# Performance work log

Hardware: AMD Instinct MI355X
Metric: run time of the kernel (lower is better)

The kernel has to match this reference:

```python
import jax, jax.numpy as jnp
import numpy as np

N_NODES = 50000
N_EDGES = 800000   # avg degree ~16
IN_CH = 128
HID = 64


def setup_inputs() -> dict:
    key = jax.random.key(0)
    k0, k1, k2, k3 = jax.random.split(key, 4)
    x = jax.random.normal(k0, (N_NODES, IN_CH), dtype=jnp.float32)
    edge_index = jax.random.randint(k1, (2, N_EDGES), 0, N_NODES, dtype=jnp.int32)
    # Glorot-ish init like torch GCNConv
    W1 = jax.random.normal(k2, (IN_CH, HID), dtype=jnp.float32) / np.sqrt(IN_CH).astype(np.float32)
    b1 = jnp.zeros((HID,), dtype=jnp.float32)
    W2 = jax.random.normal(k3, (HID, HID), dtype=jnp.float32) / np.sqrt(HID).astype(np.float32)
    b2 = jnpp = jnp.zeros((HID,), dtype=jnp.float32)
    return {"x": x, "edge_index": edge_index, "W1": W1, "b1": b1, "W2": W2, "b2": b2}


def gcn_conv(x, src, dst, W, b, n):
    """GCNConv with self-loops already appended to (src, dst).
    out = D^{-1/2} (A + I) D^{-1/2} (x @ W) + b, symmetric normalization."""
    h = x @ W                                        # [N, out]
    deg = jax.ops.segment_sum(jnp.ones(src.shape, jnp.float32), dst, num_segments=n)
    dinv = jax.lax.rsqrt(jnp.maximum(deg, 1.0))      # deg >= 1 due to self-loops
    norm = dinv[src] * dinv[dst]                     # [E+N]
    msg = h[src] * norm[:, None]                     # gather + scale
    return jax.ops.segment_sum(msg, dst, num_segments=n) + b


def reference(x, edge_index, W1, b1, W2, b2):
    n = x.shape[0]
    loop = jnp.arange(n, dtype=edge_index.dtype)
    src = jnp.concatenate([edge_index[0], loop])     # add self-loops
    dst = jnp.concatenate([edge_index[1], loop])
    # encode: GCNConv -> ReLU -> GCNConv
    z = jax.nn.relu(gcn_conv(x, src, dst, W1, b1, n))
    z = gcn_conv(z, src, dst, W2, b2, n)
    # decode: gather endpoint embeddings, elementwise product, reduce over hidden
    return (z[edge_index[0]] * z[edge_index[1]]).sum(axis=1)   # [E]
```

## Files before the change

kernel.cpp:

```cpp
#include <hip/hip_runtime.h>
#include <hip/hip_fp16.h>

#define INCH 128
#define HIDC 64
#define CAP  64

typedef int            v4i __attribute__((ext_vector_type(4)));
typedef float          v4f __attribute__((ext_vector_type(4)));
typedef unsigned int   v4u __attribute__((ext_vector_type(4)));

__device__ inline float2 u2f(unsigned int u) {
    return __half22float2(__builtin_bit_cast(__half2, u));
}
__device__ inline unsigned int f2u(float a, float b) {
    __half2 h = __float22half2_rn(make_float2(a, b));
    return __builtin_bit_cast(unsigned int, h);
}

__global__ __launch_bounds__(128, 2) void build_gemm1_kernel(const int* __restrict__ src,
                                                             const int* __restrict__ dst,
                                                             int* __restrict__ count,
                                                             unsigned short* __restrict__ col,
                                                             const float* __restrict__ x,
                                                             const float* __restrict__ W,
                                                             __half* __restrict__ hs,
                                                             int E, int N, int GB) {
    int b = (int)blockIdx.x;
    if (b >= GB) {
        int eb = b - GB;
        int g = eb & 7;
        int chunkBase = (eb >> 3) * 2048;
        int t = (int)threadIdx.x;
        if (chunkBase + 2048 <= E) {
            v4i s4[4], d4[4];
            #pragma unroll
            for (int i = 0; i < 4; ++i) {
                int e0 = chunkBase + (i * 128 + t) * 4;
                d4[i] = *(const v4i*)(dst + e0);
                s4[i] = *(const v4i*)(src + e0);
            }
            #pragma unroll
            for (int i = 0; i < 4; ++i) {
                #pragma unroll
                for (int k = 0; k < 4; ++k) {
                    int d = d4[i][k];
                    if (((d >> 4) & 7) == g) {
                        int r = atomicAdd(&count[d], 1);
                        if (r < CAP) col[(size_t)d * CAP + r] = (unsigned short)s4[i][k];
                    }
                }
            }
        } else {
            #pragma unroll
            for (int i = 0; i < 4; ++i) {
                int e0 = chunkBase + (i * 128 + t) * 4;
                for (int e = e0; e < e0 + 4 && e < E; ++e) {
                    int d = dst[e];
                    if (((d >> 4) & 7) == g) {
                        int r = atomicAdd(&count[d], 1);
                        if (r < CAP) col[(size_t)d * CAP + r] = (unsigned short)src[e];
                    }
                }
            }
        }
    } else {
        int node = (b >> 1) * 128 + (int)threadIdx.x;
        int ch0 = (b & 1) * 32;
        if (node >= N) return;
        const float4* xr = (const float4*)(x + (size_t)node * INCH);
        float acc[32];
        #pragma unroll
        for (int c = 0; c < 32; ++c) acc[c] = 0.f;
        for (int kc = 0; kc < INCH / 4; ++kc) {
            float4 xk = xr[kc];
            const float* wr = W + (kc * 4) * HIDC + ch0;
            #pragma unroll
            for (int ch = 0; ch < 32; ++ch) acc[ch] = fmaf(xk.x, wr[ch], acc[ch]);
            #pragma unroll
            for (int ch = 0; ch < 32; ++ch) acc[ch] = fmaf(xk.y, wr[HIDC + ch], acc[ch]);
            #pragma unroll
            for (int ch = 0; ch < 32; ++ch) acc[ch] = fmaf(xk.z, wr[2 * HIDC + ch], acc[ch]);
            #pragma unroll
            for (int ch = 0; ch < 32; ++ch) acc[ch] = fmaf(xk.w, wr[3 * HIDC + ch], acc[ch]);
        }
        v4u hv[4];
        #pragma unroll
        for (int k = 0; k < 4; ++k) {
            #pragma unroll
            for (int e = 0; e < 4; ++e) {
                int c2 = k * 4 + e;
                hv[k][e] = f2u(acc[2 * c2], acc[2 * c2 + 1]);
            }
        }
        v4u* hr = (v4u*)(hs + (size_t)node * HIDC + ch0);
        #pragma unroll
        for (int k = 0; k < 4; ++k) hr[k] = hv[k];
    }
}

__global__ __launch_bounds__(256) void agg1_gemm2_kernel(const int* __restrict__ count,
                                                         const unsigned short* __restrict__ col,
                                                         const __half* __restrict__ hs,
                                                         const float* __restrict__ b1,
                                                         const float* __restrict__ W2,
                                                         __half* __restrict__ out, int N) {
    __shared__ float sW2[HIDC * HIDC];
    __shared__ float sAgg[32][68];
    int t = (int)threadIdx.x;
    {
        const float4* w4 = (const float4*)W2;
        float4* s4 = (float4*)sW2;
        #pragma unroll
        for (int i = 0; i < 4; ++i) s4[t + 256 * i] = w4[t + 256 * i];
    }
    __syncthreads();

    int g = t >> 3;
    int q = t & 7;
    int node = (int)blockIdx.x * 32 + g;
    if (node >= N) return;
    int cnt = count[node];
    int deg = cnt < CAP ? cnt : CAP;
    float dn = rsqrtf((float)cnt + 1.0f);
    const v4u* z8 = (const v4u*)hs;
    v4u sf = z8[(size_t)node * 8 + q];
    float2 acc[4];
    #pragma unroll
    for (int j = 0; j < 4; ++j) {
        float2 f = u2f(sf[j]);
        acc[j] = make_float2(f.x * dn, f.y * dn);
    }
    const unsigned short* row = col + (size_t)node * CAP;
    for (int jb = 0; jb < deg; jb += 16) {
        int s[16]; int cv[16]; v4u a[16];
        #pragma unroll
        for (int u = 0; u < 16; ++u) {
            int idx = jb + u;
            s[u] = row[idx < deg ? idx : jb];
        }
        #pragma unroll
        for (int u = 0; u < 16; ++u)
            a[u] = z8[(size_t)s[u] * 8 + q];
        #pragma unroll
        for (int u = 0; u < 16; ++u)
            cv[u] = count[s[u]];
        #pragma unroll
        for (int u = 0; u < 16; ++u) {
            if (jb + u < deg) {
                float w = rsqrtf((float)cv[u] + 1.0f);
                #pragma unroll
                for (int j = 0; j < 4; ++j) {
                    float2 f = u2f(a[u][j]);
                    acc[j].x = fmaf(f.x, w, acc[j].x);
                    acc[j].y = fmaf(f.y, w, acc[j].y);
                }
            }
        }
    }
    int ch0 = q * 8;
    v4f bA = *(const v4f*)(b1 + ch0);
    v4f bB = *(const v4f*)(b1 + ch0 + 4);
    v4f pA, pB;
    #pragma unroll
    for (int j = 0; j < 4; ++j) {
        float px = fmaxf(fmaf(acc[j].x, dn, (j < 2 ? bA[2*j]   : bB[2*j-4])),   0.f);
        float py = fmaxf(fmaf(acc[j].y, dn, (j < 2 ? bA[2*j+1] : bB[2*j-3])),  0.f);
        if (j < 2) { pA[2*j] = px; pA[2*j+1] = py; }
        else       { pB[2*j-4] = px; pB[2*j-3] = py; }
    }
    *(v4f*)(&sAgg[g][ch0])     = pA;
    *(v4f*)(&sAgg[g][ch0 + 4]) = pB;
    __asm__ volatile("s_waitcnt lgkmcnt(0)" ::: "memory");

    float o[8];
    #pragma unroll
    for (int c = 0; c < 8; ++c) o[c] = 0.f;
    const float* aRow = sAgg[g];
    #pragma unroll
    for (int kk = 0; kk < 16; ++kk) {
        v4f a4 = *(const v4f*)(aRow + kk * 4);
        #pragma unroll
        for (int kv = 0; kv < 4; ++kv) {
            float av = a4[kv];
            v4f wA = *(const v4f*)(sW2 + (kk * 4 + kv) * HIDC + ch0);
            v4f wB = *(const v4f*)(sW2 + (kk * 4 + kv) * HIDC + ch0 + 4);
            #pragma unroll
            for (int c = 0; c < 4; ++c) o[c]     = fmaf(av, wA[c], o[c]);
            #pragma unroll
            for (int c = 0; c < 4; ++c) o[c + 4] = fmaf(av, wB[c], o[c + 4]);
        }
    }
    v4u hv;
    #pragma unroll
    for (int j = 0; j < 4; ++j) hv[j] = f2u(o[2*j] * dn, o[2*j+1] * dn);
    ((v4u*)out)[(size_t)node * 8 + q] = hv;
}

__global__ __launch_bounds__(256) void aggregate_kernel(const int* __restrict__ count,
                                                        const unsigned short* __restrict__ col,
                                                        const __half* __restrict__ hs,
                                                        const float* __restrict__ bias,
                                                        __half* __restrict__ agg, int N) {
    int t = (int)threadIdx.x;
    int g = t >> 3;
    int q = t & 7;
    int node = (int)blockIdx.x * 32 + g;
    if (node >= N) return;
    int cnt = count[node];
    int deg = cnt < CAP ? cnt : CAP;
    float dn = rsqrtf((float)cnt + 1.0f);
    const v4u* z8 = (const v4u*)hs;
    v4u sf = z8[(size_t)node * 8 + q];
    float2 acc[4];
    #pragma unroll
    for (int j = 0; j < 4; ++j) acc[j] = u2f(sf[j]);
    const unsigned short* row = col + (size_t)node * CAP;
    for (int jb = 0; jb < deg; jb += 16) {
        int s[16]; v4u a[16];
        #pragma unroll
        for (int u = 0; u < 16; ++u) {
            int idx = jb + u;
            s[u] = row[idx < deg ? idx : jb];
        }
        #pragma unroll
        for (int u = 0; u < 16; ++u)
            a[u] = z8[(size_t)s[u] * 8 + q];
        #pragma unroll
        for (int u = 0; u < 16; ++u) {
            if (jb + u < deg) {
                #pragma unroll
                for (int j = 0; j < 4; ++j) {
                    float2 f = u2f(a[u][j]);
                    acc[j].x += f.x;
                    acc[j].y += f.y;
                }
            }
        }
    }
    int ch0 = q * 8;
    v4f bA = *(const v4f*)(bias + ch0);
    v4f bB = *(const v4f*)(bias + ch0 + 4);
    v4u hv;
    #pragma unroll
    for (int j = 0; j < 4; ++j) {
        float bx = (j < 2) ? bA[2*j]   : bB[2*j-4];
        float by = (j < 2) ? bA[2*j+1] : bB[2*j-3];
        hv[j] = f2u(fmaf(acc[j].x, dn, bx), fmaf(acc[j].y, dn, by));
    }
    ((v4u*)agg)[(size_t)node * 8 + q] = hv;
}

__global__ __launch_bounds__(256) void decode_kernel(const int* __restrict__ src,
                                                     const int* __restrict__ dst,
                                                     const __half* __restrict__ z,
                                                     float* __restrict__ out, int E) {
    long long tid = (long long)blockIdx.x * 256 + threadIdx.x;
    int g = (int)(tid >> 3);
    int q = threadIdx.x & 7;
    int e0 = g * 8;
    if (e0 >= E) return;
    const v4u* z8 = (const v4u*)z;
    bool full = (e0 + 7 < E);
    int s[8], d[8];
    if (full) {
        v4i sv0 = __builtin_nontemporal_load((const v4i*)(src + e0));
        v4i sv1 = __builtin_nontemporal_load((const v4i*)(src + e0 + 4));
        v4i dv0 = __builtin_nontemporal_load((const v4i*)(dst + e0));
        v4i dv1 = __builtin_nontemporal_load((const v4i*)(dst + e0 + 4));
        s[0]=sv0.x; s[1]=sv0.y; s[2]=sv0.z; s[3]=sv0.w;
        s[4]=sv1.x; s[5]=sv1.y; s[6]=sv1.z; s[7]=sv1.w;
        d[0]=dv0.x; d[1]=dv0.y; d[2]=dv0.z; d[3]=dv0.w;
        d[4]=dv1.x; d[5]=dv1.y; d[6]=dv1.z; d[7]=dv1.w;
    } else {
        #pragma unroll
        for (int k = 0; k < 8; ++k) {
            int e = e0 + k < E ? e0 + k : e0;
            s[k] = src[e]; d[k] = dst[e];
        }
    }
    v4u a[8], b[8];
    #pragma unroll
    for (int k = 0; k < 8; ++k) a[k] = z8[(size_t)s[k] * 8 + q];
    #pragma unroll
    for (int k = 0; k < 8; ++k) b[k] = z8[(size_t)d[k] * 8 + q];
    float p[8];
    #pragma unroll
    for (int k = 0; k < 8; ++k) {
        float acc = 0.f;
        #pragma unroll
        for (int j = 0; j < 4; ++j) {
            float2 fa = u2f(a[k][j]);
            float2 fb = u2f(b[k][j]);
            acc = fmaf(fa.x, fb.x, acc);
            acc = fmaf(fa.y, fb.y, acc);
        }
        p[k] = acc;
    }
    #pragma unroll
    for (int m = 4; m; m >>= 1) {
        #pragma unroll
        for (int k = 0; k < 8; ++k) p[k] += __shfl_xor(p[k], m, 64);
    }
    if (q == 0) {
        if (full) {
            v4f r0; r0.x = p[0]; r0.y = p[1]; r0.z = p[2]; r0.w = p[3];
            v4f r1; r1.x = p[4]; r1.y = p[5]; r1.z = p[6]; r1.w = p[7];
            __builtin_nontemporal_store(r0, (v4f*)(out + e0));
            __builtin_nontemporal_store(r1, (v4f*)(out + e0 + 4));
        } else {
            for (int k = 0; k < 8 && e0 + k < E; ++k) out[e0 + k] = p[k];
        }
    }
}

extern "C" void kernel_launch(void* const* d_in, const int* in_sizes, int n_in,
                              void* d_out, int out_size, void* d_ws, size_t ws_size,
                              hipStream_t stream) {
    const float* x  = (const float*)d_in[0];
    const int*   ei = (const int*)d_in[1];
    const float* W1 = (const float*)d_in[2];
    const float* b1 = (const float*)d_in[3];
    const float* W2 = (const float*)d_in[4];
    const float* b2 = (const float*)d_in[5];
    float* out = (float*)d_out;

    const int hid  = in_sizes[3];
    const int inch = in_sizes[2] / hid;
    const int N    = in_sizes[0] / inch;
    const int E    = in_sizes[1] / 2;
    const int* srcp = ei;
    const int* dstp = ei + E;

    char* p = (char*)d_ws;
    auto alloc = [&](size_t bytes) { char* r = p; p += (bytes + 255) & ~(size_t)255; return r; };
    int*            count = (int*)alloc((size_t)N * 4);
    unsigned short* col   = (unsigned short*)alloc((size_t)N * CAP * 2);
    __half*         h1s   = (__half*)alloc((size_t)N * HIDC * 2);
    __half*         h2s   = (__half*)alloc((size_t)N * HIDC * 2);
    __half*         zt    = (__half*)alloc((size_t)N * HIDC * 2);

    (void)hipMemsetAsync(count, 0, (size_t)N * 4, stream);

    int GB  = 2 * ((N + 127) / 128);
    int EBK = 8 * ((E + 2047) / 2048);
    build_gemm1_kernel<<<GB + EBK, 128, 0, stream>>>(srcp, dstp, count, col,
                                                     x, W1, h1s, E, N, GB);

    agg1_gemm2_kernel<<<(N + 31) / 32, 256, 0, stream>>>(count, col, h1s, b1, W2, h2s, N);

    aggregate_kernel<<<(N + 31) / 32, 256, 0, stream>>>(count, col, h2s, b2, zt, N);

    long long groups = ((long long)E + 7) / 8;
    long long blocksD = (groups * 8 + 255) / 256;
    decode_kernel<<<(int)blocksD, 256, 0, stream>>>(srcp, dstp, zt, out, E);
}
```

Baseline: 186.5 us.

## Split hidden features into two 32-channel halves processed by separate gather passes

The node feature tables are split into two separate 32-channel half arrays (A/B), and each gather-heavy pass (aggregations and edge decode) runs once per half. Each random gather then touches a smaller working set (1.6 MB per half), so it may fit better in L2/MALL cache. The cost is more kernel launches, gathering the column indices and degree counts twice, and a read-modify-write of the output in the second decode pass. The nontemporal loads and stores in decode are also dropped.

```diff
diff --git a/kernel.cpp b/kernel.cpp
--- a/kernel.cpp
+++ b/kernel.cpp
@@ -23,7 +23,8 @@
                                                              unsigned short* __restrict__ col,
                                                              const float* __restrict__ x,
                                                              const float* __restrict__ W,
-                                                             __half* __restrict__ hs,
+                                                             __half* __restrict__ h1A,
+                                                             __half* __restrict__ h1B,
                                                              int E, int N, int GB) {
     int b = (int)blockIdx.x;
     if (b >= GB) {
@@ -92,38 +93,28 @@
                 hv[k][e] = f2u(acc[2 * c2], acc[2 * c2 + 1]);
             }
         }
-        v4u* hr = (v4u*)(hs + (size_t)node * HIDC + ch0);
+        __half* ht = (b & 1) ? h1B : h1A;
+        v4u* hr = (v4u*)(ht + (size_t)node * 32);
         #pragma unroll
         for (int k = 0; k < 4; ++k) hr[k] = hv[k];
     }
 }
 
-__global__ __launch_bounds__(256) void agg1_gemm2_kernel(const int* __restrict__ count,
-                                                         const unsigned short* __restrict__ col,
-                                                         const __half* __restrict__ hs,
-                                                         const float* __restrict__ b1,
-                                                         const float* __restrict__ W2,
-                                                         __half* __restrict__ out, int N) {
-    __shared__ float sW2[HIDC * HIDC];
-    __shared__ float sAgg[32][68];
+__global__ __launch_bounds__(256) void agg1_half_kernel(const int* __restrict__ count,
+                                                        const unsigned short* __restrict__ col,
+                                                        const __half* __restrict__ hhalf,
+                                                        const float* __restrict__ bhalf,
+                                                        __half* __restrict__ thalf, int N) {
     int t = (int)threadIdx.x;
-    {
-        const float4* w4 = (const float4*)W2;
-        float4* s4 = (float4*)sW2;
-        #pragma unroll
-        for (int i = 0; i < 4; ++i) s4[t + 256 * i] = w4[t + 256 * i];
-    }
-    __syncthreads();
-
-    int g = t >> 3;
-    int q = t & 7;
-    int node = (int)blockIdx.x * 32 + g;
+    int g = t >> 2;
+    int q = t & 3;
+    int node = (int)blockIdx.x * 64 + g;
     if (node >= N) return;
     int cnt = count[node];
     int deg = cnt < CAP ? cnt : CAP;
     float dn = rsqrtf((float)cnt + 1.0f);
-    const v4u* z8 = (const v4u*)hs;
-    v4u sf = z8[(size_t)node * 8 + q];
+    const v4u* z4 = (const v4u*)hhalf;
+    v4u sf = z4[(size_t)node * 4 + q];
     float2 acc[4];
     #pragma unroll
     for (int j = 0; j < 4; ++j) {
@@ -140,7 +131,7 @@
         }
         #pragma unroll
         for (int u = 0; u < 16; ++u)
-            a[u] = z8[(size_t)s[u] * 8 + q];
+            a[u] = z4[(size_t)s[u] * 4 + q];
         #pragma unroll
         for (int u = 0; u < 16; ++u)
             cv[u] = count[s[u]];
@@ -158,59 +149,163 @@
         }
     }
     int ch0 = q * 8;
-    v4f bA = *(const v4f*)(b1 + ch0);
-    v4f bB = *(const v4f*)(b1 + ch0 + 4);
-    v4f pA, pB;
+    v4f bA = *(const v4f*)(bhalf + ch0);
+    v4f bB = *(const v4f*)(bhalf + ch0 + 4);
+    v4u hv;
     #pragma unroll
     for (int j = 0; j < 4; ++j) {
-        float px = fmaxf(fmaf(acc[j].x, dn, (j < 2 ? bA[2*j]   : bB[2*j-4])),   0.f);
-        float py = fmaxf(fmaf(acc[j].y, dn, (j < 2 ? bA[2*j+1] : bB[2*j-3])),  0.f);
-        if (j < 2) { pA[2*j] = px; pA[2*j+1] = py; }
-        else       { pB[2*j-4] = px; pB[2*j-3] = py; }
-    }
-    *(v4f*)(&sAgg[g][ch0])     = pA;
-    *(v4f*)(&sAgg[g][ch0 + 4]) = pB;
-    __asm__ volatile("s_waitcnt lgkmcnt(0)" ::: "memory");
-
-    float o[8];
-    #pragma unroll
-    for (int c = 0; c < 8; ++c) o[c] = 0.f;
-    const float* aRow = sAgg[g];
-    #pragma unroll
-    for (int kk = 0; kk < 16; ++kk) {
-        v4f a4 = *(const v4f*)(aRow + kk * 4);
-        #pragma unroll
-        for (int kv = 0; kv < 4; ++kv) {
-            float av = a4[kv];
-            v4f wA = *(const v4f*)(sW2 + (kk * 4 + kv) * HIDC + ch0);
-            v4f wB = *(const v4f*)(sW2 + (kk * 4 + kv) * HIDC + ch0 + 4);
-            #pragma unroll
-            for (int c = 0; c < 4; ++c) o[c]     = fmaf(av, wA[c], o[c]);
-            #pragma unroll
-            for (int c = 0; c < 4; ++c) o[c + 4] = fmaf(av, wB[c], o[c + 4]);
-        }
-    }
-    v4u hv;
-    #pragma unroll
-    for (int j = 0; j < 4; ++j) hv[j] = f2u(o[2*j] * dn, o[2*j+1] * dn);
-    ((v4u*)out)[(size_t)node * 8 + q] = hv;
-}
-
-__global__ __launch_bounds__(256) void aggregate_kernel(const int* __restrict__ count,
-                                                        const unsigned short* __restrict__ col,
-                                                        const __half* __restrict__ hs,
-                                                        const float* __restrict__ bias,
-                                                        __half* __restrict__ agg, int N) {
+        float bx = (j < 2) ? bA[2*j]   : bB[2*j-4];
+        float by = (j < 2) ? bA[2*j+1] : bB[2*j-3];
+        hv[j] = f2u(fmaxf(fmaf(acc[j].x, dn, bx), 0.f),
+                    fmaxf(fmaf(acc[j].y, dn, by), 0.f));
+    }
+    ((v4u*)thalf)[(size_t)node * 4 + q] = hv;
+}
+
+__global__ __launch_bounds__(256) void agg1b_gemm2_kernel(const int* __restrict__ count,
+                                                          const unsigned short* __restrict__ col,
+                                                          const __half* __restrict__ h1B,
+                                                          const __half* __restrict__ t1A,
+                                                          const float* __restrict__ b1,
+                                                          const float* __restrict__ W2,
+                                                          __half* __restrict__ h2A,
+                                                          __half* __restrict__ h2B, int N) {
+    __shared__ float sW2[HIDC * HIDC];
+    __shared__ float sAgg[64][68];
     int t = (int)threadIdx.x;
-    int g = t >> 3;
-    int q = t & 7;
-    int node = (int)blockIdx.x * 32 + g;
+    {
+        const float4* w4 = (const float4*)W2;
+        float4* s4 = (float4*)sW2;
+        #pragma unroll
+        for (int i = 0; i < 4; ++i) s4[t + 256 * i] = w4[t + 256 * i];
+    }
+    __syncthreads();
+
+    int g = t >> 2;
+    int q = t & 3;
+    int node = (int)blockIdx.x * 64 + g;
     if (node >= N) return;
     int cnt = count[node];
     int deg = cnt < CAP ? cnt : CAP;
     float dn = rsqrtf((float)cnt + 1.0f);
-    const v4u* z8 = (const v4u*)hs;
-    v4u sf = z8[(size_t)node * 8 + q];
+    const v4u* z4 = (const v4u*)h1B;
+    v4u sf = z4[(size_t)node * 4 + q];
+    float2 acc[4];
+    #pragma unroll
+    for (int j = 0; j < 4; ++j) {
+        float2 f = u2f(sf[j]);
+        acc[j] = make_float2(f.x * dn, f.y * dn);
+    }
+    const unsigned short* row = col + (size_t)node * CAP;
+    for (int jb = 0; jb < deg; jb += 16) {
+        int s[16]; int cv[16]; v4u a[16];
+        #pragma unroll
+        for (int u = 0; u < 16; ++u) {
+            int idx = jb + u;
+            s[u] = row[idx < deg ? idx : jb];
+        }
+        #pragma unroll
+        for (int u = 0; u < 16; ++u)
+            a[u] = z4[(size_t)s[u] * 4 + q];
+        #pragma unroll
+        for (int u = 0; u < 16; ++u)
+            cv[u] = count[s[u]];
+        #pragma unroll
+        for (int u = 0; u < 16; ++u) {
+            if (jb + u < deg) {
+                float w = rsqrtf((float)cv[u] + 1.0f);
+                #pragma unroll
+                for (int j = 0; j < 4; ++j) {
+                    float2 f = u2f(a[u][j]);
+                    acc[j].x = fmaf(f.x, w, acc[j].x);
+                    acc[j].y = fmaf(f.y, w, acc[j].y);
+                }
+            }
+        }
+    }
+    int ch0 = q * 8;
+    {
+        v4f bA = *(const v4f*)(b1 + 32 + ch0);
+        v4f bB = *(const v4f*)(b1 + 32 + ch0 + 4);
+        v4f pA, pB;
+        #pragma unroll
+        for (int j = 0; j < 4; ++j) {
+            float bx = (j < 2) ? bA[2*j]   : bB[2*j-4];
+            float by = (j < 2) ? bA[2*j+1] : bB[2*j-3];
+            float px = fmaxf(fmaf(acc[j].x, dn, bx), 0.f);
+            float py = fmaxf(fmaf(acc[j].y, dn, by), 0.f);
+            if (j < 2) { pA[2*j] = px; pA[2*j+1] = py; }
+            else       { pB[2*j-4] = px; pB[2*j-3] = py; }
+        }
+        *(v4f*)(&sAgg[g][32 + ch0])     = pA;
+        *(v4f*)(&sAgg[g][32 + ch0 + 4]) = pB;
+    }
+    {
+        v4u ta = ((const v4u*)t1A)[(size_t)node * 4 + q];
+        v4f pA, pB;
+        #pragma unroll
+        for (int j = 0; j < 4; ++j) {
+            float2 f = u2f(ta[j]);
+            if (j < 2) { pA[2*j] = f.x; pA[2*j+1] = f.y; }
+            else       { pB[2*j-4] = f.x; pB[2*j-3] = f.y; }
+        }
+        *(v4f*)(&sAgg[g][ch0])     = pA;
+        *(v4f*)(&sAgg[g][ch0 + 4]) = pB;
+    }
+    __asm__ volatile("s_waitcnt lgkmcnt(0)" ::: "memory");
+
+    int oc0 = q * 16;
+    float o[16];
+    #pragma unroll
+    for (int c = 0; c < 16; ++c) o[c] = 0.f;
+    const float* aRow = sAgg[g];
+    #pragma unroll
+    for (int kk = 0; kk < 16; ++kk) {
+        v4f a4 = *(const v4f*)(aRow + kk * 4);
+        #pragma unroll
+        for (int kv = 0; kv < 4; ++kv) {
+            float av = a4[kv];
+            const float* wr = sW2 + (kk * 4 + kv) * HIDC + oc0;
+            v4f w0 = *(const v4f*)(wr);
+            v4f w1 = *(const v4f*)(wr + 4);
+            v4f w2 = *(const v4f*)(wr + 8);
+            v4f w3 = *(const v4f*)(wr + 12);
+            #pragma unroll
+            for (int c = 0; c < 4; ++c) o[c]      = fmaf(av, w0[c], o[c]);
+            #pragma unroll
+            for (int c = 0; c < 4; ++c) o[c + 4]  = fmaf(av, w1[c], o[c + 4]);
+            #pragma unroll
+            for (int c = 0; c < 4; ++c) o[c + 8]  = fmaf(av, w2[c], o[c + 8]);
+            #pragma unroll
+            for (int c = 0; c < 4; ++c) o[c + 12] = fmaf(av, w3[c], o[c + 12]);
+        }
+    }
+    v4u hv0, hv1;
+    #pragma unroll
+    for (int j = 0; j < 4; ++j) hv0[j] = f2u(o[2*j] * dn,     o[2*j+1] * dn);
+    #pragma unroll
+    for (int j = 0; j < 4; ++j) hv1[j] = f2u(o[8+2*j] * dn,   o[8+2*j+1] * dn);
+    __half* hb = (q < 2) ? h2A : h2B;
+    v4u* hr = (v4u*)(hb + (size_t)node * 32) + (q & 1) * 2;
+    hr[0] = hv0;
+    hr[1] = hv1;
+}
+
+__global__ __launch_bounds__(256) void agg2_half_kernel(const int* __restrict__ count,
+                                                        const unsigned short* __restrict__ col,
+                                                        const __half* __restrict__ hhalf,
+                                                        const float* __restrict__ bhalf,
+                                                        __half* __restrict__ zhalf, int N) {
+    int t = (int)threadIdx.x;
+    int g = t >> 2;
+    int q = t & 3;
+    int node = (int)blockIdx.x * 64 + g;
+    if (node >= N) return;
+    int cnt = count[node];
+    int deg = cnt < CAP ? cnt : CAP;
+    float dn = rsqrtf((float)cnt + 1.0f);
+    const v4u* z4 = (const v4u*)hhalf;
+    v4u sf = z4[(size_t)node * 4 + q];
     float2 acc[4];
     #pragma unroll
     for (int j = 0; j < 4; ++j) acc[j] = u2f(sf[j]);
@@ -224,7 +319,7 @@
         }
         #pragma unroll
         for (int u = 0; u < 16; ++u)
-            a[u] = z8[(size_t)s[u] * 8 + q];
+            a[u] = z4[(size_t)s[u] * 4 + q];
         #pragma unroll
         for (int u = 0; u < 16; ++u) {
             if (jb + u < deg) {
@@ -238,8 +333,8 @@
         }
     }
     int ch0 = q * 8;
-    v4f bA = *(const v4f*)(bias + ch0);
-    v4f bB = *(const v4f*)(bias + ch0 + 4);
+    v4f bA = *(const v4f*)(bhalf + ch0);
+    v4f bB = *(const v4f*)(bhalf + ch0 + 4);
     v4u hv;
     #pragma unroll
     for (int j = 0; j < 4; ++j) {
@@ -247,26 +342,27 @@
         float by = (j < 2) ? bA[2*j+1] : bB[2*j-3];
         hv[j] = f2u(fmaf(acc[j].x, dn, bx), fmaf(acc[j].y, dn, by));
     }
-    ((v4u*)agg)[(size_t)node * 8 + q] = hv;
-}
-
-__global__ __launch_bounds__(256) void decode_kernel(const int* __restrict__ src,
-                                                     const int* __restrict__ dst,
-                                                     const __half* __restrict__ z,
-                                                     float* __restrict__ out, int E) {
+    ((v4u*)zhalf)[(size_t)node * 4 + q] = hv;
+}
+
+template<int ADD>
+__global__ __launch_bounds__(256) void decode_half_kernel(const int* __restrict__ src,
+                                                          const int* __restrict__ dst,
+                                                          const __half* __restrict__ zhalf,
+                                                          float* __restrict__ out, int E) {
     long long tid = (long long)blockIdx.x * 256 + threadIdx.x;
-    int g = (int)(tid >> 3);
-    int q = threadIdx.x & 7;
+    int g = (int)(tid >> 2);
+    int q = threadIdx.x & 3;
     int e0 = g * 8;
     if (e0 >= E) return;
-    const v4u* z8 = (const v4u*)z;
+    const v4u* z4 = (const v4u*)zhalf;
     bool full = (e0 + 7 < E);
     int s[8], d[8];
     if (full) {
-        v4i sv0 = __builtin_nontemporal_load((const v4i*)(src + e0));
-        v4i sv1 = __builtin_nontemporal_load((const v4i*)(src + e0 + 4));
-        v4i dv0 = __builtin_nontemporal_load((const v4i*)(dst + e0));
-        v4i dv1 = __builtin_nontemporal_load((const v4i*)(dst + e0 + 4));
+        v4i sv0 = *(const v4i*)(src + e0);
+        v4i sv1 = *(const v4i*)(src + e0 + 4);
+        v4i dv0 = *(const v4i*)(dst + e0);
+        v4i dv1 = *(const v4i*)(dst + e0 + 4);
         s[0]=sv0.x; s[1]=sv0.y; s[2]=sv0.z; s[3]=sv0.w;
         s[4]=sv1.x; s[5]=sv1.y; s[6]=sv1.z; s[7]=sv1.w;
         d[0]=dv0.x; d[1]=dv0.y; d[2]=dv0.z; d[3]=dv0.w;
@@ -280,9 +376,9 @@
     }
     v4u a[8], b[8];
     #pragma unroll
-    for (int k = 0; k < 8; ++k) a[k] = z8[(size_t)s[k] * 8 + q];
-    #pragma unroll
-    for (int k = 0; k < 8; ++k) b[k] = z8[(size_t)d[k] * 8 + q];
+    for (int k = 0; k < 8; ++k) a[k] = z4[(size_t)s[k] * 4 + q];
+    #pragma unroll
+    for (int k = 0; k < 8; ++k) b[k] = z4[(size_t)d[k] * 4 + q];
     float p[8];
     #pragma unroll
     for (int k = 0; k < 8; ++k) {
@@ -297,18 +393,29 @@
         p[k] = acc;
     }
     #pragma unroll
-    for (int m = 4; m; m >>= 1) {
+    for (int m = 2; m; m >>= 1) {
         #pragma unroll
         for (int k = 0; k < 8; ++k) p[k] += __shfl_xor(p[k], m, 64);
     }
     if (q == 0) {
         if (full) {
-            v4f r0; r0.x = p[0]; r0.y = p[1]; r0.z = p[2]; r0.w = p[3];
-            v4f r1; r1.x = p[4]; r1.y = p[5]; r1.z = p[6]; r1.w = p[7];
-            __builtin_nontemporal_store(r0, (v4f*)(out + e0));
-            __builtin_nontemporal_store(r1, (v4f*)(out + e0 + 4));
+            v4f r0, r1;
+            if (ADD) {
+                r0 = *(const v4f*)(out + e0);
+                r1 = *(const v4f*)(out + e0 + 4);
+                #pragma unroll
+                for (int k = 0; k < 4; ++k) { r0[k] += p[k]; r1[k] += p[k+4]; }
+            } else {
+                #pragma unroll
+                for (int k = 0; k < 4; ++k) { r0[k] = p[k]; r1[k] = p[k+4]; }
+            }
+            *(v4f*)(out + e0)     = r0;
+            *(v4f*)(out + e0 + 4) = r1;
         } else {
-            for (int k = 0; k < 8 && e0 + k < E; ++k) out[e0 + k] = p[k];
+            for (int k = 0; k < 8 && e0 + k < E; ++k) {
+                if (ADD) out[e0 + k] += p[k];
+                else     out[e0 + k]  = p[k];
+            }
         }
     }
 }
@@ -335,22 +442,30 @@
     auto alloc = [&](size_t bytes) { char* r = p; p += (bytes + 255) & ~(size_t)255; return r; };
     int*            count = (int*)alloc((size_t)N * 4);
     unsigned short* col   = (unsigned short*)alloc((size_t)N * CAP * 2);
-    __half*         h1s   = (__half*)alloc((size_t)N * HIDC * 2);
-    __half*         h2s   = (__half*)alloc((size_t)N * HIDC * 2);
-    __half*         zt    = (__half*)alloc((size_t)N * HIDC * 2);
+    __half*         h1A   = (__half*)alloc((size_t)N * 32 * 2);
+    __half*         h1B   = (__half*)alloc((size_t)N * 32 * 2);
+    __half*         t1A   = (__half*)alloc((size_t)N * 32 * 2);
+    __half*         h2A   = (__half*)alloc((size_t)N * 32 * 2);
+    __half*         h2B   = (__half*)alloc((size_t)N * 32 * 2);
+    __half*         zA    = (__half*)alloc((size_t)N * 32 * 2);
+    __half*         zB    = (__half*)alloc((size_t)N * 32 * 2);
 
     (void)hipMemsetAsync(count, 0, (size_t)N * 4, stream);
 
     int GB  = 2 * ((N + 127) / 128);
     int EBK = 8 * ((E + 2047) / 2048);
     build_gemm1_kernel<<<GB + EBK, 128, 0, stream>>>(srcp, dstp, count, col,
-                                                     x, W1, h1s, E, N, GB);
-
-    agg1_gemm2_kernel<<<(N + 31) / 32, 256, 0, stream>>>(count, col, h1s, b1, W2, h2s, N);
-
-    aggregate_kernel<<<(N + 31) / 32, 256, 0, stream>>>(count, col, h2s, b2, zt, N);
+                                                     x, W1, h1A, h1B, E, N, GB);
+
+    int AB = (N + 63) / 64;
+    agg1_half_kernel<<<AB, 256, 0, stream>>>(count, col, h1A, b1, t1A, N);
+    agg1b_gemm2_kernel<<<AB, 256, 0, stream>>>(count, col, h1B, t1A, b1, W2,
+                                               h2A, h2B, N);
+    agg2_half_kernel<<<AB, 256, 0, stream>>>(count, col, h2A, b2,      zA, N);
+    agg2_half_kernel<<<AB, 256, 0, stream>>>(count, col, h2B, b2 + 32, zB, N);
 
     long long groups = ((long long)E + 7) / 8;
-    long long blocksD = (groups * 8 + 255) / 256;
-    decode_kernel<<<(int)blocksD, 256, 0, stream>>>(srcp, dstp, zt, out, E);
-}
+    long long blocksD = (groups * 4 + 255) / 256;
+    decode_half_kernel<0><<<(int)blocksD, 256, 0, stream>>>(srcp, dstp, zA, out, E);
+    decode_half_kernel<1><<<(int)blocksD, 256, 0, stream>>>(srcp, dstp, zB, out, E);
+}
```

New measurement: 219.7 us. +17.8%, slower.
